# Performance work log

Measured on AMD Instinct MI355X. Metric: run time of the kernel, lower is better.

The kernel has to match this reference:

```python
import jax, jax.numpy as jnp
import numpy as np

N, E, H, B, L = 100000, 600000, 128, 512, 10


def setup_inputs() -> dict:
    key = jax.random.key(0)
    ks = jax.random.split(key, 16)
    def lin(k, fan_in, fan_out):
        return (jax.random.normal(k, (fan_in, fan_out), jnp.float32) / np.sqrt(fan_in)).astype(jnp.float32)
    inp = {
        'node_reps_0': jax.random.normal(ks[0], (N, H), jnp.float32),
        'node_reps_1': jax.random.normal(ks[1], (N, H), jnp.float32),
        'W1': lin(ks[2], 2 * H, 4 * H), 'b1': jnp.zeros((4 * H,), jnp.float32),
        'W2': lin(ks[3], 4 * H, 2 * H), 'b2': jnp.zeros((2 * H,), jnp.float32),
        'W3': lin(ks[4], 2 * H, H),     'b3': jnp.zeros((H,), jnp.float32),
        'W4': lin(ks[5], H, H),         'b4': jnp.zeros((H,), jnp.float32),
        'W5': lin(ks[6], H, L),         'b5': jnp.zeros((L,), jnp.float32),
        'edge_index': jax.random.randint(ks[7], (2, E), 0, N, jnp.int64 if jax.config.jax_enable_x64 else jnp.int32),
        'batch': jnp.sort(jax.random.randint(ks[8], (N,), 0, B)),
        'y': jax.random.randint(ks[9], (B,), 0, L),
    }
    return inp


def reference(node_reps_0, node_reps_1, W1, b1, W2, b2, W3, b3, W4, b4, W5, b5,
              edge_index, batch, y):
    # ava_node_reps = reps(full graph) - reps(occupied subgraph)
    reps = node_reps_0 - node_reps_1                      # [N, H]
    src, dst = edge_index[0], edge_index[1]               # [E]
    # gather endpoints, concat -> edge action rep MLP (ELU)
    a = jnp.concatenate([reps[src], reps[dst]], axis=1)   # [E, 2H]
    h = jax.nn.elu(a @ W1 + b1)                           # [E, 4H]
    h = jax.nn.elu(h @ W2 + b2)                           # [E, 2H]
    h = h @ W3 + b3                                       # [E, H]
    # edge action prob generator: h -> h -> num_labels
    logits = jax.nn.elu(h @ W4 + b4) @ W5 + b5            # [E, L]
    edge_batch = batch[src]                               # [E] graph id per edge
    target_y = y[edge_batch]                              # [E]
    scores = jnp.take_along_axis(logits, target_y[:, None], axis=1)[:, 0]  # [E]
    # segment-wise (per-graph) softmax over available edges
    seg_max = jax.ops.segment_max(scores, edge_batch, num_segments=B)
    ex = jnp.exp(scores - seg_max[edge_batch])
    seg_sum = jax.ops.segment_sum(ex, edge_batch, num_segments=B)
    probs = ex / seg_sum[edge_batch]                      # [E]
    # scatter_max: per-graph max prob and its (first) argmax edge index
    added_probs = jax.ops.segment_max(probs, edge_batch, num_segments=B)  # [B]
    idx = jnp.arange(E, dtype=edge_batch.dtype)
    cand = jnp.where(probs == added_probs[edge_batch], idx, E)
    added_actions = jax.ops.segment_min(cand, edge_batch, num_segments=B)  # [B]
    return probs, added_probs, added_actions
```

## Files before the change

### kernel.cpp

```cpp
#include <hip/hip_runtime.h>
#include <hip/hip_bf16.h>
#include <cmath>

#define NN 100000
#define EE 600000
#define BB 512
#define LL 10

typedef __attribute__((ext_vector_type(8))) short  bf16x8;
typedef __attribute__((ext_vector_type(4))) float  f32x4;
typedef unsigned int uint;
typedef unsigned short ushort;
typedef unsigned long long u64;

__device__ __forceinline__ float elu_f(float x){ return x > 0.f ? x : __expf(x) - 1.f; }

__device__ __forceinline__ ushort bf16_rne(float f){
  uint u = __float_as_uint(f);
  return (ushort)((u + 0x7FFFu + ((u >> 16) & 1u)) >> 16);
}

__device__ __forceinline__ f32x4 MFMA(bf16x8 a, bf16x8 b, f32x4 c){
  return __builtin_amdgcn_mfma_f32_16x16x32_bf16(a, b, c, 0, 0, 0);
}

__device__ __forceinline__ unsigned enc_f(float f){
  unsigned u = __float_as_uint(f);
  return (u & 0x80000000u) ? ~u : (u | 0x80000000u);
}
__device__ __forceinline__ float dec_f(unsigned u){
  return (u & 0x80000000u) ? __uint_as_float(u ^ 0x80000000u) : __uint_as_float(~u);
}
#define ENC_NEG_INF 0x007FFFFFu

#define AROW 260

__global__ __launch_bounds__(256) void kReps(const float* __restrict__ r0,
                                             const float* __restrict__ r1,
                                             ushort* __restrict__ repsF){
  int gid = blockIdx.x*256 + threadIdx.x;
  int n = gid >> 4, k8 = gid & 15;
  const float4* a = (const float4*)(r0 + (size_t)n*128 + k8*8);
  const float4* b = (const float4*)(r1 + (size_t)n*128 + k8*8);
  float4 x0 = a[0], x1 = a[1], y0 = b[0], y1 = b[1];
  float d[8] = {x0.x-y0.x, x0.y-y0.y, x0.z-y0.z, x0.w-y0.w,
                x1.x-y1.x, x1.y-y1.y, x1.z-y1.z, x1.w-y1.w};
  ushort hi[8], lo[8];
  #pragma unroll
  for (int j=0;j<8;++j){
    hi[j] = bf16_rne(d[j]);
    float fh = __uint_as_float(((uint)hi[j])<<16);
    lo[j] = bf16_rne(d[j] - fh);
  }
  ushort* dh = repsF + (size_t)n*256 + k8*8;
  ushort* dl = dh + 128;
  #pragma unroll
  for (int j=0;j<8;++j){ dh[j] = hi[j]; dl[j] = lo[j]; }
}

__global__ __launch_bounds__(256) void kPrepW(const float* __restrict__ W, int N,
                                              int KT, int NT, ushort* __restrict__ dst){
  int gid = blockIdx.x*256 + threadIdx.x;
  int total = KT*NT*64;
  if (gid >= total) return;
  int l = gid & 63, tile = gid >> 6;
  int kt = tile / NT, nt = tile % NT;
  int kbase = kt*32 + (l>>4)*8;
  int n = nt*16 + (l&15);
  int partStride = KT*NT*512;
  int base = tile*512 + l*8;
  #pragma unroll
  for (int j=0;j<8;++j){
    float f = W[(size_t)(kbase+j)*N + n];
    ushort h = bf16_rne(f);
    float fh = __uint_as_float(((uint)h)<<16);
    dst[base + j] = h;
    dst[partStride + base + j] = bf16_rne(f - fh);
  }
}

template<int NTILES>
__device__ __forceinline__ void xposeN(ushort* sT, const f32x4* Cg,
                                       const float* __restrict__ biasPtr,
                                       bool doElu, int l){
  const int quad = l >> 4, r16 = l & 15;
  uint* ldsu = (uint*)sT;
  #pragma unroll
  for (int i = 0; i < NTILES; ++i){
    float bv = biasPtr[i*16 + r16];
    #pragma unroll
    for (int mtl = 0; mtl < 2; ++mtl){
      f32x4 v = Cg[i*2 + mtl];
      ushort hi[4], lo[4];
      #pragma unroll
      for (int r = 0; r < 4; ++r){
        float f = v[r] + bv;
        if (doElu) f = elu_f(f);
        hi[r] = bf16_rne(f);
        float fh = __uint_as_float(((uint)hi[r]) << 16);
        lo[r] = bf16_rne(f - fh);
      }
      uint v01h = (uint)hi[0] | ((uint)hi[1]<<16);
      uint v23h = (uint)hi[2] | ((uint)hi[3]<<16);
      uint v01l = (uint)lo[0] | ((uint)lo[1]<<16);
      uint v23l = (uint)lo[2] | ((uint)lo[3]<<16);
      uint t01h = __shfl_xor(v01h,1), t23h = __shfl_xor(v23h,1);
      uint t01l = __shfl_xor(v01l,1), t23l = __shfl_xor(v23l,1);
      int c2 = (i*16 + (r16 & ~1)) >> 1;
      int m0 = mtl*16 + quad*4;
      if (!(l & 1)){
        ldsu[(m0+0)*34 + c2]        = (v01h & 0xFFFFu) | (t01h << 16);
        ldsu[(m0+1)*34 + c2]        = (v01h >> 16) | (t01h & 0xFFFF0000u);
        ldsu[1088 + (m0+0)*34 + c2] = (v01l & 0xFFFFu) | (t01l << 16);
        ldsu[1088 + (m0+1)*34 + c2] = (v01l >> 16) | (t01l & 0xFFFF0000u);
      } else {
        ldsu[(m0+2)*34 + c2]        = (t23h & 0xFFFFu) | (v23h << 16);
        ldsu[(m0+3)*34 + c2]        = (t23h >> 16) | (v23h & 0xFFFF0000u);
        ldsu[1088 + (m0+2)*34 + c2] = (t23l & 0xFFFFu) | (v23l << 16);
        ldsu[1088 + (m0+3)*34 + c2] = (t23l >> 16) | (v23l & 0xFFFF0000u);
      }
    }
  }
}

__device__ __forceinline__ bf16x8 readA(const ushort* region, int part, int m, int colBase){
  union { uint2 u[2]; bf16x8 v; } cvt;
  const ushort* p = region + part*2176 + m*68 + colBase;
  cvt.u[0] = *(const uint2*)p;
  cvt.u[1] = *(const uint2*)(p + 4);
  return cvt.v;
}

__device__ __forceinline__ bf16x8 loadA8(const ushort* p){
  union { uint2 u[2]; bf16x8 v; } cvt;
  cvt.u[0] = *(const uint2*)p;
  cvt.u[1] = *(const uint2*)(p + 4);
  return cvt.v;
}

__device__ __forceinline__ void produceSlice(int s, int w, int l, int quad, int r16,
    const ushort* sA,
    const ushort* __restrict__ W1F, const float* __restrict__ b1,
    ushort* buf){
  f32x4 C1[2];
  C1[0] = (f32x4)0.f; C1[1] = (f32x4)0.f;
  #pragma unroll
  for (int hk = 0; hk < 8; ++hk){
    const int rbase = (hk < 4) ? 0 : 32;
    const int ko = (hk & 3)*32 + quad*8;
    const ushort* r0p = sA + (rbase + r16)*AROW + ko;
    const ushort* r1p = sA + (rbase + 16 + r16)*AROW + ko;
    bf16x8 Ah0 = loadA8(r0p);
    bf16x8 Al0 = loadA8(r0p + 128);
    bf16x8 Ah1 = loadA8(r1p);
    bf16x8 Al1 = loadA8(r1p + 128);
    const bf16x8* WfH = (const bf16x8*)W1F + ((size_t)hk*32 + s*4 + w)*64 + l;
    const bf16x8* WfL = WfH + 8*32*64;
    bf16x8 Bh = WfH[0], Bl = WfL[0];
    C1[0] = MFMA(Ah0, Bh, C1[0]); C1[1] = MFMA(Ah1, Bh, C1[1]);
    C1[0] = MFMA(Ah0, Bl, C1[0]); C1[1] = MFMA(Ah1, Bl, C1[1]);
    C1[0] = MFMA(Al0, Bh, C1[0]); C1[1] = MFMA(Al1, Bh, C1[1]);
  }
  xposeN<1>(buf + w*16, C1, b1 + s*64 + w*16, true, l);
}

__device__ __forceinline__ void consumeSlice(int s, int w, int l, int quad, int r16,
    const ushort* buf, const ushort* __restrict__ W2F, f32x4 (&C2q)[8]){
  #pragma unroll
  for (int j2 = 0; j2 < 2; ++j2){
    int colBase = j2*32 + quad*8;
    bf16x8 Ah[2], Al[2];
    #pragma unroll
    for (int mtl = 0; mtl < 2; ++mtl){
      int m = mtl*16 + r16;
      Ah[mtl] = readA(buf, 0, m, colBase);
      Al[mtl] = readA(buf, 1, m, colBase);
    }
    const int kt = s*2 + j2;
    const bf16x8* WfH = (const bf16x8*)W2F + ((size_t)kt*16 + w*4)*64 + l;
    const bf16x8* WfL = WfH + 16*16*64;
    #pragma unroll
    for (int j = 0; j < 4; ++j){
      bf16x8 Bh = WfH[j*64], Bl = WfL[j*64];
      f32x4 c0 = C2q[j*2], c1 = C2q[j*2+1];
      c0 = MFMA(Ah[0], Bh, c0); c1 = MFMA(Ah[1], Bh, c1);
      c0 = MFMA(Ah[0], Bl, c0); c1 = MFMA(Ah[1], Bl, c1);
      c0 = MFMA(Al[0], Bh, c0); c1 = MFMA(Al[1], Bh, c1);
      C2q[j*2] = c0; C2q[j*2+1] = c1;
    }
  }
}

__global__ __launch_bounds__(256, 3) void kMLP(
    const ushort* __restrict__ repsF,
    const ushort* __restrict__ W1F, const ushort* __restrict__ W2F,
    const ushort* __restrict__ W3F, const ushort* __restrict__ W4F,
    const float* __restrict__ b1, const float* __restrict__ b2,
    const float* __restrict__ b3, const float* __restrict__ b4,
    const float* __restrict__ W5, const float* __restrict__ b5,
    const int* __restrict__ edge_index, const int* __restrict__ batch,
    const int* __restrict__ y,
    float* __restrict__ scores, int* __restrict__ ebatch)
{
  __shared__ __align__(16) ushort sReg01[2*4352];
  __shared__ __align__(16) ushort sA[64*AROW];
  __shared__ int sTy[32];
  __shared__ int sNode[64];
  __shared__ float sRed[4][32];

  const int tid = threadIdx.x;
  const int w = tid >> 6;
  const int l = tid & 63;
  const int quad = l >> 4, r16 = l & 15;
  const int e0 = blockIdx.x * 32;

  if (tid < 32){
    int s = edge_index[e0 + tid];
    int d = edge_index[EE + e0 + tid];
    sNode[tid] = s;
    sNode[32 + tid] = d;
    int eb = batch[s];
    ebatch[e0 + tid] = eb;
    sTy[tid] = y[eb];
  }
  __syncthreads();

  #pragma unroll
  for (int k = 0; k < 8; ++k){
    int c = tid + k*256;
    int row = c >> 5, col = c & 31;
    const ushort* src = repsF + (size_t)sNode[row]*256 + col*8;
    uint4 v = *(const uint4*)src;
    ushort* dst = sA + row*AROW + col*8;
    *(uint2*)dst        = make_uint2(v.x, v.y);
    *(uint2*)(dst + 4)  = make_uint2(v.z, v.w);
  }
  __syncthreads();

  f32x4 C2q[8];
  #pragma unroll
  for (int i=0;i<8;++i) C2q[i] = (f32x4)0.f;

  produceSlice(0, w, l, quad, r16, sA, W1F, b1, sReg01);
  __syncthreads();
  #pragma unroll 1
  for (int s = 0; s < 7; ++s){
    produceSlice(s+1, w, l, quad, r16, sA, W1F, b1, sReg01 + ((s+1)&1)*4352);
    consumeSlice(s, w, l, quad, r16, sReg01 + (s&1)*4352, W2F, C2q);
    __syncthreads();
  }
  consumeSlice(7, w, l, quad, r16, sReg01 + 4352, W2F, C2q);
  __syncthreads();

  ushort* regW = (w < 2) ? (sReg01 + w*4352) : (sA + (w-2)*4352);
  xposeN<4>(regW, C2q, b2 + w*64, true, l);
  __syncthreads();

  f32x4 C3q[4];
  #pragma unroll
  for (int i=0;i<4;++i) C3q[i] = (f32x4)0.f;
  #pragma unroll
  for (int kt = 0; kt < 8; ++kt){
    int rw = kt >> 1;
    const ushort* reg = (rw < 2) ? (sReg01 + rw*4352) : (sA + (rw-2)*4352);
    int colBase = (kt & 1)*32 + quad*8;
    bf16x8 Ah[2], Al[2];
    #pragma unroll
    for (int mtl = 0; mtl < 2; ++mtl){
      int m = mtl*16 + r16;
      Ah[mtl] = readA(reg, 0, m, colBase);
      Al[mtl] = readA(reg, 1, m, colBase);
    }
    const bf16x8* WfH = (const bf16x8*)W3F + ((size_t)kt*8 + w*2)*64 + l;
    const bf16x8* WfL = WfH + 8*8*64;
    #pragma unroll
    for (int j = 0; j < 2; ++j){
      bf16x8 Bh = WfH[j*64], Bl = WfL[j*64];
      f32x4 c0 = C3q[j*2], c1 = C3q[j*2+1];
      c0 = MFMA(Ah[0], Bh, c0); c1 = MFMA(Ah[1], Bh, c1);
      c0 = MFMA(Ah[0], Bl, c0); c1 = MFMA(Ah[1], Bl, c1);
      c0 = MFMA(Al[0], Bh, c0); c1 = MFMA(Al[1], Bh, c1);
      C3q[j*2] = c0; C3q[j*2+1] = c1;
    }
  }
  __syncthreads();

  xposeN<2>(sReg01 + (w>>1)*4352 + (w&1)*32, C3q, b3 + w*32, false, l);
  __syncthreads();

  f32x4 C4q[4];
  #pragma unroll
  for (int i=0;i<4;++i) C4q[i] = (f32x4)0.f;
  #pragma unroll
  for (int kt = 0; kt < 4; ++kt){
    const ushort* reg = sReg01 + (kt>>1)*4352;
    int colBase = (kt & 1)*32 + quad*8;
    bf16x8 Ah[2], Al[2];
    #pragma unroll
    for (int mtl = 0; mtl < 2; ++mtl){
      int m = mtl*16 + r16;
      Ah[mtl] = readA(reg, 0, m, colBase);
      Al[mtl] = readA(reg, 1, m, colBase);
    }
    const bf16x8* WfH = (const bf16x8*)W4F + ((size_t)kt*8 + w*2)*64 + l;
    const bf16x8* WfL = WfH + 4*8*64;
    #pragma unroll
    for (int j = 0; j < 2; ++j){
      bf16x8 Bh = WfH[j*64], Bl = WfL[j*64];
      f32x4 c0 = C4q[j*2], c1 = C4q[j*2+1];
      c0 = MFMA(Ah[0], Bh, c0); c1 = MFMA(Ah[1], Bh, c1);
      c0 = MFMA(Ah[0], Bl, c0); c1 = MFMA(Ah[1], Bl, c1);
      c0 = MFMA(Al[0], Bh, c0); c1 = MFMA(Al[1], Bh, c1);
      C4q[j*2] = c0; C4q[j*2+1] = c1;
    }
  }

  int tvals[2][4];
  #pragma unroll
  for (int mtl=0;mtl<2;++mtl)
    #pragma unroll
    for (int r=0;r<4;++r) tvals[mtl][r] = sTy[mtl*16 + quad*4 + r];

  float p[2][4] = {{0.f,0.f,0.f,0.f},{0.f,0.f,0.f,0.f}};
  #pragma unroll
  for (int j = 0; j < 2; ++j){
    int n4 = (w*2 + j)*16 + r16;
    float bv = b4[n4];
    const float* w5r = W5 + n4*LL;
    #pragma unroll
    for (int mtl = 0; mtl < 2; ++mtl){
      f32x4 c = C4q[j*2+mtl];
      #pragma unroll
      for (int r=0;r<4;++r)
        p[mtl][r] += elu_f(c[r] + bv) * w5r[tvals[mtl][r]];
    }
  }
  #pragma unroll
  for (int d = 8; d >= 1; d >>= 1){
    #pragma unroll
    for (int mtl=0;mtl<2;++mtl)
      #pragma unroll
      for (int r=0;r<4;++r)
        p[mtl][r] += __shfl_down(p[mtl][r], d, 16);
  }
  if (r16 == 0){
    #pragma unroll
    for (int mtl=0;mtl<2;++mtl)
      #pragma unroll
      for (int r=0;r<4;++r){
        int m = mtl*16 + quad*4 + r;
        sRed[w][m] = p[mtl][r];
      }
  }
  __syncthreads();
  if (tid < 32){
    float s = sRed[0][tid] + sRed[1][tid] + sRed[2][tid] + sRed[3][tid];
    scores[e0 + tid] = s + b5[sTy[tid]];
  }
}

__global__ void kInitSeg(unsigned* segmax, float* segsum, u64* gkey){
  int b = blockIdx.x*blockDim.x + threadIdx.x;
  if (b < BB){ segmax[b] = ENC_NEG_INF; segsum[b] = 0.f; gkey[b] = ~0ull; }
}

__global__ __launch_bounds__(256) void kSegMax(const float* __restrict__ scores,
                                               const int* __restrict__ eb,
                                               unsigned* __restrict__ segmax){
  __shared__ unsigned l[BB];
  for (int b = threadIdx.x; b < BB; b += 256) l[b] = 0u;
  __syncthreads();
  for (int e = blockIdx.x*256 + threadIdx.x; e < EE; e += gridDim.x*256)
    atomicMax(&l[eb[e]], enc_f(scores[e]));
  __syncthreads();
  for (int b = threadIdx.x; b < BB; b += 256)
    if (l[b]) atomicMax(&segmax[b], l[b]);
}

__global__ __launch_bounds__(256) void kExpSum(const float* __restrict__ scores,
                                               const int* __restrict__ eb,
                                               const unsigned* __restrict__ segmax,
                                               float* __restrict__ segsum,
                                               float* __restrict__ outprobs){
  __shared__ float l[BB];
  for (int b = threadIdx.x; b < BB; b += 256) l[b] = 0.f;
  __syncthreads();
  for (int e = blockIdx.x*256 + threadIdx.x; e < EE; e += gridDim.x*256){
    int b = eb[e];
    float ex = expf(scores[e] - dec_f(segmax[b]));
    outprobs[e] = ex;
    atomicAdd(&l[b], ex);
  }
  __syncthreads();
  for (int b = threadIdx.x; b < BB; b += 256)
    if (l[b] != 0.f) atomicAdd(&segsum[b], l[b]);
}

__global__ __launch_bounds__(256) void kMaxArg(float* __restrict__ outprobs,
                                               const int* __restrict__ eb,
                                               const float* __restrict__ segsum,
                                               u64* __restrict__ gkey){
  __shared__ u64 l[BB];
  for (int b = threadIdx.x; b < BB; b += 256) l[b] = ~0ull;
  __syncthreads();
  for (int e = blockIdx.x*256 + threadIdx.x; e < EE; e += gridDim.x*256){
    int b = eb[e];
    float p = outprobs[e] / segsum[b];
    outprobs[e] = p;
    u64 key = ((u64)(~enc_f(p)) << 32) | (unsigned)e;
    atomicMin(&l[b], key);
  }
  __syncthreads();
  for (int b = threadIdx.x; b < BB; b += 256)
    if (l[b] != ~0ull) atomicMin(&gkey[b], l[b]);
}

__global__ void kFinal(const u64* __restrict__ gkey, float* __restrict__ out){
  int b = threadIdx.x;
  if (b < BB){
    u64 k = gkey[b];
    unsigned enc = ~(unsigned)(k >> 32);
    out[EE + b]      = dec_f(enc);
    out[EE + BB + b] = (float)(unsigned)(k & 0xFFFFFFFFu);
  }
}

extern "C" void kernel_launch(void* const* d_in, const int* in_sizes, int n_in,
                              void* d_out, int out_size, void* d_ws, size_t ws_size,
                              hipStream_t stream){
  const float* r0 = (const float*)d_in[0];
  const float* r1 = (const float*)d_in[1];
  const float* W1 = (const float*)d_in[2];
  const float* b1 = (const float*)d_in[3];
  const float* W2 = (const float*)d_in[4];
  const float* b2 = (const float*)d_in[5];
  const float* W3 = (const float*)d_in[6];
  const float* b3 = (const float*)d_in[7];
  const float* W4 = (const float*)d_in[8];
  const float* b4 = (const float*)d_in[9];
  const float* W5 = (const float*)d_in[10];
  const float* b5 = (const float*)d_in[11];
  const int* edge_index = (const int*)d_in[12];
  const int* batch = (const int*)d_in[13];
  const int* y = (const int*)d_in[14];
  float* out = (float*)d_out;

  char* ws = (char*)d_ws;
  size_t off = 0;
  float*    scores = (float*)(ws + off);    off += (size_t)EE*4;
  int*      ebatch = (int*)(ws + off);      off += (size_t)EE*4;
  unsigned* segmax = (unsigned*)(ws + off); off += BB*4;
  float*    segsum = (float*)(ws + off);    off += BB*4;
  off = (off + 7) & ~(size_t)7;
  u64*      gkey   = (u64*)(ws + off);      off += BB*8;
  off = (off + 511) & ~(size_t)511;
  ushort* repsF = (ushort*)(ws + off);      off += (size_t)NN*256*2;
  ushort* W1F   = (ushort*)(ws + off);      off += (size_t)2*8*32*512*2;
  ushort* W2F   = (ushort*)(ws + off);      off += (size_t)2*16*16*512*2;
  ushort* W3F   = (ushort*)(ws + off);      off += (size_t)2*8*8*512*2;
  ushort* W4F   = (ushort*)(ws + off);      off += (size_t)2*4*8*512*2;

  kInitSeg<<<2, 256, 0, stream>>>(segmax, segsum, gkey);
  kReps<<<(NN*16)/256, 256, 0, stream>>>(r0, r1, repsF);
  kPrepW<<<(8*32*64)/256, 256, 0, stream>>>(W1, 512, 8, 32, W1F);
  kPrepW<<<(16*16*64)/256, 256, 0, stream>>>(W2, 256, 16, 16, W2F);
  kPrepW<<<(8*8*64)/256, 256, 0, stream>>>(W3, 128, 8, 8, W3F);
  kPrepW<<<(4*8*64)/256, 256, 0, stream>>>(W4, 128, 4, 8, W4F);

  kMLP<<<EE/32, 256, 0, stream>>>(repsF, W1F, W2F, W3F, W4F,
                                  b1, b2, b3, b4, W5, b5,
                                  edge_index, batch, y, scores, ebatch);

  kSegMax<<<256, 256, 0, stream>>>(scores, ebatch, segmax);
  kExpSum<<<256, 256, 0, stream>>>(scores, ebatch, segmax, segsum, out);
  kMaxArg<<<256, 256, 0, stream>>>(out, ebatch, segsum, gkey);
  kFinal <<<1, 512, 0, stream>>>(gkey, out);
}
```

Baseline: 1.418 ms.

## Fuse segment softmax epilogue into one cooperative kernel with grid syncs

Replaces the four separate epilogue launches (segment max, exp-sum, max/argmax, final) with a single cooperative kernel. Grid-wide syncs separate the phases, and a shared-memory buffer is reused across them. The aim is to remove kernel launch gaps and per-launch overhead for these small reduction passes. The cost is the grid.sync barriers, plus the requirement that all 256 blocks be co-resident; if the cooperative launch fails, the code falls back to the old kernels.

Measured after the change: 1.511 ms. +6.6%, slower.

```diff
diff --git a/kernel.cpp b/kernel.cpp
--- a/kernel.cpp
+++ b/kernel.cpp
@@ -1,6 +1,9 @@
 #include <hip/hip_runtime.h>
 #include <hip/hip_bf16.h>
+#include <hip/hip_cooperative_groups.h>
 #include <cmath>
+
+namespace cg = cooperative_groups;
 
 #define NN 100000
 #define EE 600000
@@ -364,6 +367,65 @@
   if (b < BB){ segmax[b] = ENC_NEG_INF; segsum[b] = 0.f; gkey[b] = ~0ull; }
 }
 
+__global__ __launch_bounds__(256) void kEpilogue(const float* __restrict__ scores,
+                                                 const int* __restrict__ eb,
+                                                 unsigned* __restrict__ segmax,
+                                                 float* __restrict__ segsum,
+                                                 u64* __restrict__ gkey,
+                                                 float* __restrict__ out){
+  cg::grid_group grid = cg::this_grid();
+  __shared__ __align__(8) u64 lsk[BB];
+  unsigned* lsu = (unsigned*)lsk;
+  float*    lsf = (float*)lsk;
+  const int tid = threadIdx.x;
+  const int stride = gridDim.x*256;
+
+  for (int b = tid; b < BB; b += 256) lsu[b] = 0u;
+  __syncthreads();
+  for (int e = blockIdx.x*256 + tid; e < EE; e += stride)
+    atomicMax(&lsu[eb[e]], enc_f(scores[e]));
+  __syncthreads();
+  for (int b = tid; b < BB; b += 256)
+    if (lsu[b]) atomicMax(&segmax[b], lsu[b]);
+  grid.sync();
+
+  for (int b = tid; b < BB; b += 256) lsf[b] = 0.f;
+  __syncthreads();
+  for (int e = blockIdx.x*256 + tid; e < EE; e += stride){
+    int b = eb[e];
+    float ex = expf(scores[e] - dec_f(segmax[b]));
+    out[e] = ex;
+    atomicAdd(&lsf[b], ex);
+  }
+  __syncthreads();
+  for (int b = tid; b < BB; b += 256)
+    if (lsf[b] != 0.f) atomicAdd(&segsum[b], lsf[b]);
+  grid.sync();
+
+  for (int b = tid; b < BB; b += 256) lsk[b] = ~0ull;
+  __syncthreads();
+  for (int e = blockIdx.x*256 + tid; e < EE; e += stride){
+    int b = eb[e];
+    float p = out[e] / segsum[b];
+    out[e] = p;
+    u64 key = ((u64)(~enc_f(p)) << 32) | (unsigned)e;
+    atomicMin(&lsk[b], key);
+  }
+  __syncthreads();
+  for (int b = tid; b < BB; b += 256)
+    if (lsk[b] != ~0ull) atomicMin(&gkey[b], lsk[b]);
+  grid.sync();
+
+  if (blockIdx.x == 0){
+    for (int b = tid; b < BB; b += 256){
+      u64 k = gkey[b];
+      unsigned enc = ~(unsigned)(k >> 32);
+      out[EE + b]      = dec_f(enc);
+      out[EE + BB + b] = (float)(unsigned)(k & 0xFFFFFFFFu);
+    }
+  }
+}
+
 __global__ __launch_bounds__(256) void kSegMax(const float* __restrict__ scores,
                                                const int* __restrict__ eb,
                                                unsigned* __restrict__ segmax){
@@ -471,8 +533,19 @@
                                   b1, b2, b3, b4, W5, b5,
                                   edge_index, batch, y, scores, ebatch);
 
-  kSegMax<<<256, 256, 0, stream>>>(scores, ebatch, segmax);
-  kExpSum<<<256, 256, 0, stream>>>(scores, ebatch, segmax, segsum, out);
-  kMaxArg<<<256, 256, 0, stream>>>(out, ebatch, segsum, gkey);
-  kFinal <<<1, 512, 0, stream>>>(gkey, out);
-}
+  {
+    const float* scoresC = scores;
+    const int*   ebC     = ebatch;
+    void* args[] = { (void*)&scoresC, (void*)&ebC, (void*)&segmax,
+                     (void*)&segsum, (void*)&gkey, (void*)&out };
+    hipError_t err = hipLaunchCooperativeKernel((const void*)kEpilogue,
+                                                dim3(256), dim3(256),
+                                                args, 0, stream);
+    if (err != hipSuccess){
+      kSegMax<<<256, 256, 0, stream>>>(scores, ebatch, segmax);
+      kExpSum<<<256, 256, 0, stream>>>(scores, ebatch, segmax, segsum, out);
+      kMaxArg<<<256, 256, 0, stream>>>(out, ebatch, segsum, gkey);
+      kFinal <<<1, 512, 0, stream>>>(gkey, out);
+    }
+  }
+}
```
